# Kernel tuning notes

Measured on AMD Instinct MI355X. Metric: run time of the kernel, lower is better.

## Reference

```python
import jax, jax.numpy as jnp
import numpy as np

B, S, D, H = 2, 4096, 512, 8
DK = D // H
NEG = -9e15


def setup_inputs() -> dict:
    key = jax.random.key(0)
    ks = jax.random.split(key, 8)
    scale = 1.0 / np.sqrt(D)
    return {
        "q": jax.random.normal(ks[0], (B, S, D), jnp.float32),
        "k": jax.random.normal(ks[1], (B, S, D), jnp.float32),
        "v": jax.random.normal(ks[2], (B, S, D), jnp.float32),
        "mask": jnp.ones((1, 1, S, S), jnp.int32),
        "w_q": jax.random.normal(ks[3], (D, D), jnp.float32) * scale,
        "w_k": jax.random.normal(ks[4], (D, D), jnp.float32) * scale,
        "w_v": jax.random.normal(ks[5], (D, D), jnp.float32) * scale,
        "w_o": jax.random.normal(ks[6], (D, D), jnp.float32) * scale,
        "b_o": jnp.zeros((D,), jnp.float32),
    }


def reference(q, k, v, mask, w_q, w_k, w_v, w_o, b_o):
    # projections (nn.Linear: x @ W.T); split heads -> [B, H, S, DK]
    def split(x, w):
        return (x @ w.T).reshape(B, S, H, DK).transpose(0, 2, 1, 3)

    qh, kh, vh = split(q, w_q), split(k, w_k), split(v, w_v)
    scores = jnp.einsum("bhqd,bhkd->bhqk", qh, kh) / np.sqrt(DK)
    scores = jnp.where(mask == 0, NEG, scores)
    attn = jax.nn.softmax(scores, axis=-1)  # dropout p=0.0 (eval)
    out = jnp.einsum("bhqk,bhkd->bhqd", attn, vh)
    out = out.transpose(0, 2, 1, 3).reshape(B, S, D)
    return out @ w_o.T + b_o
```

## Files before the change

### kernel.cpp

```cpp
#include <hip/hip_runtime.h>
#include <hip/hip_fp16.h>

typedef _Float16 f16;
typedef _Float16 f16x2 __attribute__((ext_vector_type(2)));
typedef _Float16 f16x4v __attribute__((ext_vector_type(4)));
typedef _Float16 f16x8 __attribute__((ext_vector_type(8)));
typedef float f32x4 __attribute__((ext_vector_type(4)));
typedef float f32x16 __attribute__((ext_vector_type(16)));
typedef float fvec4 __attribute__((ext_vector_type(4)));
typedef unsigned int uint4v __attribute__((ext_vector_type(4)));

typedef f16x8 f16x8m __attribute__((may_alias));
typedef f16x4v f16x4m __attribute__((may_alias));

static constexpr int BB = 2, SS = 4096, DD = 512, HH = 8, DKK = 64;
static constexpr int MM = BB * SS;
static constexpr int NSPLIT = 2;
static constexpr int KVB = 32;
static constexpr int NT2 = SS / NSPLIT / KVB;
static constexpr float LOG2E = 1.4426950408889634f;
static constexpr float SMAX = 12.0f;

#define MFMA_F16(a, b, c) __builtin_amdgcn_mfma_f32_16x16x32_f16((a), (b), (c), 0, 0, 0)
#define MFMA32(a, b, c) __builtin_amdgcn_mfma_f32_32x32x16_f16((a), (b), (c), 0, 0, 0)

#define CVT_PKU(a, b) __builtin_bit_cast(unsigned, __builtin_amdgcn_cvt_pkrtz((a), (b)))

#define GLOAD16(gp, lp)                                                        \
  __builtin_amdgcn_global_load_lds(                                            \
      (const __attribute__((address_space(1))) void*)(const void*)(gp),        \
      (__attribute__((address_space(3))) void*)(lp), 16, 0, 0)

__global__ __launch_bounds__(256, 2) void proj3(
    const float* __restrict__ Aq, const float* __restrict__ Ak,
    const float* __restrict__ Av, const float* __restrict__ Wq,
    const float* __restrict__ Wk, const float* __restrict__ Wv,
    f16* __restrict__ Oq, f16* __restrict__ Ok, f16* __restrict__ Ov,
    float alq) {
  __shared__ __align__(16) f16 Al[2][128 * 32];
  __shared__ __align__(16) f16 Bl[2][128 * 32];

  const float* A32;
  const float* W;
  f16* Outp;
  float alpha;
  if (blockIdx.z == 0) {
    A32 = Aq; W = Wq; Outp = Oq; alpha = alq;
  } else if (blockIdx.z == 1) {
    A32 = Ak; W = Wk; Outp = Ok; alpha = 1.0f;
  } else {
    A32 = Av; W = Wv; Outp = Ov; alpha = 1.0f;
  }

  const int tid = threadIdx.x;
  const int lane = tid & 63;
  const int wave = tid >> 6;
  const int wm = wave >> 1, wn = wave & 1;
  const int cq = lane & 15, g = lane >> 4;
  const int bm = blockIdx.x, bn = blockIdx.y;

  f16x8 ar[2], br[2];

  auto loadStage = [&](int ks) {
#pragma unroll
    for (int i = 0; i < 2; ++i) {
      const int c = tid + 256 * i;
      const int row = c >> 2, cc = c & 3;
      const int k = ks * 32 + cc * 8;
      const float* p = A32 + (size_t)(bm * 128 + row) * DD + k;
      fvec4 x0 = *(const fvec4*)p;
      fvec4 x1 = *(const fvec4*)(p + 4);
      f16x8 h;
#pragma unroll
      for (int j = 0; j < 4; ++j) { h[j] = (f16)x0[j]; h[4 + j] = (f16)x1[j]; }
      ar[i] = h;
      const float* wp = W + (size_t)(bn * 128 + row) * DD + k;
      fvec4 y0 = *(const fvec4*)wp;
      fvec4 y1 = *(const fvec4*)(wp + 4);
      f16x8 hw;
#pragma unroll
      for (int j = 0; j < 4; ++j) { hw[j] = (f16)y0[j]; hw[4 + j] = (f16)y1[j]; }
      br[i] = hw;
    }
  };
  auto writeStage = [&](int bf) {
#pragma unroll
    for (int i = 0; i < 2; ++i) {
      const int c = tid + 256 * i;
      const int row = c >> 2, cc = c & 3;
      const int off = row * 32 + ((cc ^ (row & 3)) * 8);
      *(f16x8m*)&Al[bf][off] = ar[i];
      *(f16x8m*)&Bl[bf][off] = br[i];
    }
  };

  f32x4 acc[4][4] = {};
  loadStage(0);
  writeStage(0);
  __syncthreads();

  for (int ks = 0; ks < 16; ++ks) {
    const int bf = ks & 1;
    if (ks < 15) loadStage(ks + 1);
    f16x8 af[4], bfr[4];
#pragma unroll
    for (int f = 0; f < 4; ++f) {
      const int arow = wm * 64 + f * 16 + cq;
      af[f] = *(const f16x8m*)&Al[bf][arow * 32 + ((g ^ (arow & 3)) * 8)];
      const int brow = wn * 64 + f * 16 + cq;
      bfr[f] = *(const f16x8m*)&Bl[bf][brow * 32 + ((g ^ (brow & 3)) * 8)];
    }
#pragma unroll
    for (int fm = 0; fm < 4; ++fm)
#pragma unroll
      for (int fn = 0; fn < 4; ++fn)
        acc[fm][fn] = MFMA_F16(af[fm], bfr[fn], acc[fm][fn]);
    if (ks < 15) writeStage(bf ^ 1);
    __syncthreads();
  }

  const int rowb = bm * 128 + wm * 64;
  const int colb = bn * 128 + wn * 64;
#pragma unroll
  for (int fn = 0; fn < 4; ++fn) {
    const int col = colb + fn * 16 + cq;
#pragma unroll
    for (int fm = 0; fm < 4; ++fm) {
      const f32x4 v = acc[fm][fn];
#pragma unroll
      for (int r = 0; r < 4; ++r) {
        const int row = rowb + fm * 16 + 4 * g + r;
        const int b = row >> 12, s = row & 4095;
        const int h = col >> 6, dk = col & 63;
        Outp[(((size_t)(b * HH + h)) * SS + s) * DKK + dk] = (f16)(v[r] * alpha);
      }
    }
  }
}

__global__ __launch_bounds__(256, 2) void gemm_out(const f16* __restrict__ A16,
                                                   const float* __restrict__ W,
                                                   float* __restrict__ Out,
                                                   const float* __restrict__ bias) {
  __shared__ __align__(16) f16 Al[2][128 * 32];
  __shared__ __align__(16) f16 Bl[2][128 * 32];

  const int tid = threadIdx.x;
  const int lane = tid & 63;
  const int wave = tid >> 6;
  const int wm = wave >> 1, wn = wave & 1;
  const int cq = lane & 15, g = lane >> 4;
  const int bm = blockIdx.x, bn = blockIdx.y;

  f16x8 ar[2], br[2];
  auto loadStage = [&](int ks) {
#pragma unroll
    for (int i = 0; i < 2; ++i) {
      const int c = tid + 256 * i;
      const int row = c >> 2, cc = c & 3;
      const int k = ks * 32 + cc * 8;
      ar[i] = *(const f16x8*)(A16 + (size_t)(bm * 128 + row) * DD + k);
      const float* wp = W + (size_t)(bn * 128 + row) * DD + k;
      fvec4 y0 = *(const fvec4*)wp;
      fvec4 y1 = *(const fvec4*)(wp + 4);
      f16x8 hw;
#pragma unroll
      for (int j = 0; j < 4; ++j) { hw[j] = (f16)y0[j]; hw[4 + j] = (f16)y1[j]; }
      br[i] = hw;
    }
  };
  auto writeStage = [&](int bf) {
#pragma unroll
    for (int i = 0; i < 2; ++i) {
      const int c = tid + 256 * i;
      const int row = c >> 2, cc = c & 3;
      const int off = row * 32 + ((cc ^ (row & 3)) * 8);
      *(f16x8m*)&Al[bf][off] = ar[i];
      *(f16x8m*)&Bl[bf][off] = br[i];
    }
  };

  f32x4 acc[4][4] = {};
  loadStage(0);
  writeStage(0);
  __syncthreads();

  for (int ks = 0; ks < 16; ++ks) {
    const int bf = ks & 1;
    if (ks < 15) loadStage(ks + 1);
    f16x8 af[4], bfr[4];
#pragma unroll
    for (int f = 0; f < 4; ++f) {
      const int arow = wm * 64 + f * 16 + cq;
      af[f] = *(const f16x8m*)&Al[bf][arow * 32 + ((g ^ (arow & 3)) * 8)];
      const int brow = wn * 64 + f * 16 + cq;
      bfr[f] = *(const f16x8m*)&Bl[bf][brow * 32 + ((g ^ (brow & 3)) * 8)];
    }
#pragma unroll
    for (int fm = 0; fm < 4; ++fm)
#pragma unroll
      for (int fn = 0; fn < 4; ++fn)
        acc[fm][fn] = MFMA_F16(af[fm], bfr[fn], acc[fm][fn]);
    if (ks < 15) writeStage(bf ^ 1);
    __syncthreads();
  }

  const int rowb = bm * 128 + wm * 64;
  const int colb = bn * 128 + wn * 64;
#pragma unroll
  for (int fn = 0; fn < 4; ++fn) {
    const int col = colb + fn * 16 + cq;
    const float bb = bias[col];
#pragma unroll
    for (int fm = 0; fm < 4; ++fm) {
      const f32x4 v = acc[fm][fn];
#pragma unroll
      for (int r = 0; r < 4; ++r) {
        const int row = rowb + fm * 16 + 4 * g + r;
        Out[(size_t)row * DD + col] = v[r] + bb;
      }
    }
  }
}

__global__ __launch_bounds__(256) void transpose_v(const f16* __restrict__ Vh,
                                                   f16* __restrict__ Vt) {
  __shared__ __align__(16) f16 T[64][72];
  const int tid = threadIdx.x;
  const int bh = blockIdx.y;
  const int s0 = blockIdx.x * 64;
#pragma unroll
  for (int i = 0; i < 2; ++i) {
    const int c = tid + 256 * i;
    const int r = c >> 3, ch = c & 7;
    f16x8 v = *(const f16x8*)(Vh + ((size_t)bh * SS + s0 + r) * DKK + ch * 8);
#pragma unroll
    for (int j = 0; j < 8; ++j) T[r][ch * 8 + j] = v[j];
  }
  __syncthreads();
#pragma unroll
  for (int i = 0; i < 2; ++i) {
    const int c = tid + 256 * i;
    const int d = c >> 3, ch = c & 7;
    f16x4v lo, hi4;
#pragma unroll
    for (int j = 0; j < 4; ++j) lo[j] = T[ch * 8 + j][d];
#pragma unroll
    for (int j = 0; j < 4; ++j) hi4[j] = T[ch * 8 + 4 + j][d];
    f16* dst = Vt + ((size_t)bh * DKK + d) * SS + s0 + 16 * (ch >> 1) + 4 * (ch & 1);
    *(f16x4m*)dst = lo;
    *(f16x4m*)(dst + 8) = hi4;
  }
}

__global__ __launch_bounds__(256, 2) void attn_fwd(const f16* __restrict__ Qh,
                                                   const f16* __restrict__ Kh,
                                                   const f16* __restrict__ Vt,
                                                   f16* __restrict__ O) {
  __shared__ __align__(16) char smem[65536];

  const int tid = threadIdx.x, lane = tid & 63, wave = tid >> 6;
  const int q32 = lane & 31, hi = lane >> 5;
  const int e = wave & 1;
  const int sp = wave >> 1;
  const int bh = blockIdx.x & 15;
  const int qi = blockIdx.x >> 4;
  const int qrow0 = qi * 128 + e * 64;

  const f16* Qb = Qh + (size_t)bh * SS * DKK;
  const f16* Kb = Kh + (size_t)bh * SS * DKK;
  const f16* Vb = Vt + (size_t)bh * DKK * SS;

  char* const pb = smem + wave * 16384;
  f16* const pb16 = (f16*)pb;

  f16x8 qf0[4], qf1[4];
#pragma unroll
  for (int s = 0; s < 4; ++s) {
    qf0[s] = *(const f16x8*)(Qb + (size_t)(qrow0 + q32) * DKK + s * 16 + hi * 8);
    qf1[s] =
        *(const f16x8*)(Qb + (size_t)(qrow0 + 32 + q32) * DKK + s * 16 + hi * 8);
  }

  const f16* kRd[4];
#pragma unroll
  for (int s = 0; s < 4; ++s)
    kRd[s] = (const f16*)(pb + q32 * 128 + (((2 * s + hi) ^ (q32 & 7)) * 16));
  const f16* vRdA[2];
  const f16* vRdB[2];
#pragma unroll
  for (int s = 0; s < 2; ++s) {
    vRdA[s] = (const f16*)(pb + 8192 + q32 * 64 + (((2 * s + hi) ^ (q32 & 3)) * 16));
    vRdB[s] =
        (const f16*)(pb + 8192 + (32 + q32) * 64 + (((2 * s + hi) ^ (q32 & 3)) * 16));
  }

  const int rsub = lane >> 3;
  const int jsrc = (lane & 7) ^ rsub;
  const int r16 = lane >> 2;
  const int jsrcV = (lane & 3) ^ (r16 & 3);
  const int kvb0 = sp * (SS / NSPLIT);

  const f16* kS = Kb + (size_t)(kvb0 + rsub) * DKK + jsrc * 8;
  const f16* vS = Vb + (size_t)r16 * SS + kvb0 + jsrcV * 8;

  f16* const kDst = pb16;
  f16* const vDst = pb16 + 4096;

  auto stage = [&](int par) {
#pragma unroll
    for (int i = 0; i < 4; ++i)
      GLOAD16(kS + (size_t)i * 8 * DKK, kDst + par + i * 512);
#pragma unroll
    for (int i = 0; i < 4; ++i)
      GLOAD16(vS + (size_t)i * 16 * SS, vDst + par + i * 512);
    kS += KVB * DKK;
    vS += KVB;
  };

  f32x16 CINIT;
#pragma unroll
  for (int i = 0; i < 16; ++i) CINIT[i] = -SMAX;
  const f16 one1 = (f16)1.0f;
  const f16x8 ones = {one1, one1, one1, one1, one1, one1, one1, one1};

  f32x16 oacc00 = {}, oacc01 = {};
  f32x16 oacc10 = {}, oacc11 = {};
  f32x16 lacc0 = {}, lacc1 = {};

  struct PF { f16x8 s[2]; };
  PF pf0, pf1;

  stage(0);

  auto body = [&](int kt, int par) {
    if (kt < NT2 - 1) {
      stage(par ^ 2048);
      asm volatile("s_waitcnt vmcnt(8)" ::: "memory");
    } else {
      asm volatile("s_waitcnt vmcnt(0)" ::: "memory");
    }

    __builtin_amdgcn_s_setprio(1);
    f16x8 kf0 = *(const f16x8m*)(kRd[0] + par);
    f16x8 kf1 = *(const f16x8m*)(kRd[1] + par);
    f16x8 kf2 = *(const f16x8m*)(kRd[2] + par);
    f16x8 kf3 = *(const f16x8m*)(kRd[3] + par);
    f32x16 sc0 = MFMA32(kf0, qf0[0], CINIT);
    f32x16 sc1 = MFMA32(kf0, qf1[0], CINIT);
    sc0 = MFMA32(kf1, qf0[1], sc0);
    sc1 = MFMA32(kf1, qf1[1], sc1);
    sc0 = MFMA32(kf2, qf0[2], sc0);
    sc1 = MFMA32(kf2, qf1[2], sc1);
    sc0 = MFMA32(kf3, qf0[3], sc0);
    sc1 = MFMA32(kf3, qf1[3], sc1);
    __builtin_amdgcn_s_setprio(0);

#pragma unroll
    for (int i = 0; i < 16; ++i) sc0[i] = __builtin_amdgcn_exp2f(sc0[i]);
    unsigned dw[4];
#pragma unroll
    for (int s = 0; s < 2; ++s) {
#pragma unroll
      for (int m = 0; m < 4; ++m) {
        const int u = 2 * s + (m >> 1), c = m & 1;
        dw[m] = CVT_PKU(sc0[4 * u + 2 * c], sc0[4 * u + 2 * c + 1]);
      }
      uint4v uu = {dw[0], dw[1], dw[2], dw[3]};
      pf0.s[s] = __builtin_bit_cast(f16x8, uu);
    }
#pragma unroll
    for (int i = 0; i < 16; ++i) sc1[i] = __builtin_amdgcn_exp2f(sc1[i]);
#pragma unroll
    for (int s = 0; s < 2; ++s) {
#pragma unroll
      for (int m = 0; m < 4; ++m) {
        const int u = 2 * s + (m >> 1), c = m & 1;
        dw[m] = CVT_PKU(sc1[4 * u + 2 * c], sc1[4 * u + 2 * c + 1]);
      }
      uint4v uu = {dw[0], dw[1], dw[2], dw[3]};
      pf1.s[s] = __builtin_bit_cast(f16x8, uu);
    }

    __builtin_amdgcn_s_setprio(1);
#pragma unroll
    for (int s = 0; s < 2; ++s) {
      const f16x8 vA = *(const f16x8m*)(vRdA[s] + par);
      const f16x8 vB = *(const f16x8m*)(vRdB[s] + par);
      oacc00 = MFMA32(vA, pf0.s[s], oacc00);
      oacc01 = MFMA32(vB, pf0.s[s], oacc01);
      oacc10 = MFMA32(vA, pf1.s[s], oacc10);
      oacc11 = MFMA32(vB, pf1.s[s], oacc11);
      lacc0 = MFMA32(ones, pf0.s[s], lacc0);
      lacc1 = MFMA32(ones, pf1.s[s], lacc1);
    }
    __builtin_amdgcn_s_setprio(0);
  };

  for (int t = 0; t < NT2 / 2; ++t) {
    body(2 * t, 0);
    body(2 * t + 1, 2048);
  }

  float lr0 = lacc0[0], lr1 = lacc1[0];
  __syncthreads();
  float* const cbuf = (float*)smem;
  const int ci = (e * 64 + lane) * 67;
  if (sp == 1) {
#pragma unroll
    for (int i = 0; i < 16; ++i) {
      cbuf[ci + i] = oacc00[i];
      cbuf[ci + 16 + i] = oacc01[i];
      cbuf[ci + 33 + i] = oacc10[i];
      cbuf[ci + 49 + i] = oacc11[i];
    }
    cbuf[ci + 32] = lr0;
    cbuf[ci + 65] = lr1;
  }
  __syncthreads();
  if (sp == 0) {
#pragma unroll
    for (int i = 0; i < 16; ++i) {
      oacc00[i] += cbuf[ci + i];
      oacc01[i] += cbuf[ci + 16 + i];
      oacc10[i] += cbuf[ci + 33 + i];
      oacc11[i] += cbuf[ci + 49 + i];
    }
    lr0 += cbuf[ci + 32];
    lr1 += cbuf[ci + 65];

    const float inv0 = 1.f / lr0;
    const float inv1 = 1.f / lr1;
    const int b = bh >> 3, h = bh & 7;
#pragma unroll
    for (int g = 0; g < 2; ++g) {
      const float inv = g ? inv1 : inv0;
      const f32x16& oa = g ? oacc10 : oacc00;
      const f32x16& ob = g ? oacc11 : oacc01;
      const int srow = qrow0 + g * 32 + q32;
      f16* Orow = O + ((size_t)(b * SS + srow)) * DD + h * DKK;
#pragma unroll
      for (int u = 0; u < 4; ++u) {
        f16x4v o0, o1;
#pragma unroll
        for (int r = 0; r < 4; ++r) {
          o0[r] = (f16)(oa[4 * u + r] * inv);
          o1[r] = (f16)(ob[4 * u + r] * inv);
        }
        *(f16x4m*)(Orow + 8 * u + 4 * hi) = o0;
        *(f16x4m*)(Orow + 32 + 8 * u + 4 * hi) = o1;
      }
    }
  }
}

extern "C" void kernel_launch(void* const* d_in, const int* in_sizes, int n_in,
                              void* d_out, int out_size, void* d_ws,
                              size_t ws_size, hipStream_t stream) {
  const float* q = (const float*)d_in[0];
  const float* k = (const float*)d_in[1];
  const float* v = (const float*)d_in[2];
  const float* w_q = (const float*)d_in[4];
  const float* w_k = (const float*)d_in[5];
  const float* w_v = (const float*)d_in[6];
  const float* w_o = (const float*)d_in[7];
  const float* b_o = (const float*)d_in[8];
  float* out = (float*)d_out;

  char* ws = (char*)d_ws;
  const size_t SZ = (size_t)MM * DD * sizeof(f16);
  f16* Qh = (f16*)(ws + 0 * SZ);
  f16* Kh = (f16*)(ws + 1 * SZ);
  f16* Vh = (f16*)(ws + 2 * SZ);
  f16* Vt = (f16*)(ws + 3 * SZ);
  f16* Ob = (f16*)(ws + 4 * SZ);

  proj3<<<dim3(MM / 128, DD / 128, 3), 256, 0, stream>>>(
      q, k, v, w_q, w_k, w_v, Qh, Kh, Vh, 0.125f * LOG2E);
  transpose_v<<<dim3(SS / 64, BB * HH), 256, 0, stream>>>(Vh, Vt);
  attn_fwd<<<dim3(32 * BB * HH), 256, 0, stream>>>(Qh, Kh, Vt, Ob);
  gemm_out<<<dim3(MM / 128, DD / 128), 256, 0, stream>>>(Ob, w_o, out, b_o);
}
```

Baseline: 141.5 us.

## Share K/V LDS tiles between wave pairs and process two tiles per barrier

```diff
diff --git a/kernel.cpp b/kernel.cpp
--- a/kernel.cpp
+++ b/kernel.cpp
@@ -271,7 +271,7 @@
   const f16* Kb = Kh + (size_t)bh * SS * DKK;
   const f16* Vb = Vt + (size_t)bh * DKK * SS;
 
-  char* const pb = smem + wave * 16384;
+  char* const pb = smem + sp * 32768;
   f16* const pb16 = (f16*)pb;
 
   f16x8 qf0[4], qf1[4];
@@ -290,9 +290,10 @@
   const f16* vRdB[2];
 #pragma unroll
   for (int s = 0; s < 2; ++s) {
-    vRdA[s] = (const f16*)(pb + 8192 + q32 * 64 + (((2 * s + hi) ^ (q32 & 3)) * 16));
-    vRdB[s] =
-        (const f16*)(pb + 8192 + (32 + q32) * 64 + (((2 * s + hi) ^ (q32 & 3)) * 16));
+    vRdA[s] =
+        (const f16*)(pb + 16384 + q32 * 64 + (((2 * s + hi) ^ (q32 & 3)) * 16));
+    vRdB[s] = (const f16*)(pb + 16384 + (32 + q32) * 64 +
+                           (((2 * s + hi) ^ (q32 & 3)) * 16));
   }
 
   const int rsub = lane >> 3;
@@ -301,19 +302,19 @@
   const int jsrcV = (lane & 3) ^ (r16 & 3);
   const int kvb0 = sp * (SS / NSPLIT);
 
-  const f16* kS = Kb + (size_t)(kvb0 + rsub) * DKK + jsrc * 8;
-  const f16* vS = Vb + (size_t)r16 * SS + kvb0 + jsrcV * 8;
-
-  f16* const kDst = pb16;
-  f16* const vDst = pb16 + 4096;
-
-  auto stage = [&](int par) {
-#pragma unroll
-    for (int i = 0; i < 4; ++i)
-      GLOAD16(kS + (size_t)i * 8 * DKK, kDst + par + i * 512);
-#pragma unroll
-    for (int i = 0; i < 4; ++i)
-      GLOAD16(vS + (size_t)i * 16 * SS, vDst + par + i * 512);
+  const f16* kS = Kb + (size_t)(kvb0 + e * 16 + rsub) * DKK + jsrc * 8;
+  const f16* vS = Vb + (size_t)(e * 32 + r16) * SS + kvb0 + jsrcV * 8;
+
+  f16* const kDst0 = pb16 + (e * 16) * 64;
+  f16* const kDst1 = pb16 + (e * 16 + 8) * 64;
+  f16* const vDst0 = pb16 + 8192 + (e * 32) * 32;
+  f16* const vDst1 = pb16 + 8192 + (e * 32 + 16) * 32;
+
+  auto stage = [&](int slot) {
+    GLOAD16(kS, kDst0 + slot);
+    GLOAD16(kS + 8 * DKK, kDst1 + slot);
+    GLOAD16(vS, vDst0 + slot);
+    GLOAD16(vS + 16 * SS, vDst1 + slot);
     kS += KVB * DKK;
     vS += KVB;
   };
@@ -328,78 +329,109 @@
   f32x16 oacc10 = {}, oacc11 = {};
   f32x16 lacc0 = {}, lacc1 = {};
 
-  struct PF { f16x8 s[2]; };
-  PF pf0, pf1;
-
-  stage(0);
-
-  auto body = [&](int kt, int par) {
-    if (kt < NT2 - 1) {
-      stage(par ^ 2048);
-      asm volatile("s_waitcnt vmcnt(8)" ::: "memory");
-    } else {
-      asm volatile("s_waitcnt vmcnt(0)" ::: "memory");
-    }
-
-    __builtin_amdgcn_s_setprio(1);
-    f16x8 kf0 = *(const f16x8m*)(kRd[0] + par);
-    f16x8 kf1 = *(const f16x8m*)(kRd[1] + par);
-    f16x8 kf2 = *(const f16x8m*)(kRd[2] + par);
-    f16x8 kf3 = *(const f16x8m*)(kRd[3] + par);
-    f32x16 sc0 = MFMA32(kf0, qf0[0], CINIT);
-    f32x16 sc1 = MFMA32(kf0, qf1[0], CINIT);
-    sc0 = MFMA32(kf1, qf0[1], sc0);
-    sc1 = MFMA32(kf1, qf1[1], sc1);
-    sc0 = MFMA32(kf2, qf0[2], sc0);
-    sc1 = MFMA32(kf2, qf1[2], sc1);
-    sc0 = MFMA32(kf3, qf0[3], sc0);
-    sc1 = MFMA32(kf3, qf1[3], sc1);
-    __builtin_amdgcn_s_setprio(0);
-
-#pragma unroll
-    for (int i = 0; i < 16; ++i) sc0[i] = __builtin_amdgcn_exp2f(sc0[i]);
+  auto softpack = [&](f32x16& sc, f16x8* pf) {
+#pragma unroll
+    for (int i = 0; i < 16; ++i) sc[i] = __builtin_amdgcn_exp2f(sc[i]);
     unsigned dw[4];
 #pragma unroll
     for (int s = 0; s < 2; ++s) {
 #pragma unroll
       for (int m = 0; m < 4; ++m) {
         const int u = 2 * s + (m >> 1), c = m & 1;
-        dw[m] = CVT_PKU(sc0[4 * u + 2 * c], sc0[4 * u + 2 * c + 1]);
+        dw[m] = CVT_PKU(sc[4 * u + 2 * c], sc[4 * u + 2 * c + 1]);
       }
       uint4v uu = {dw[0], dw[1], dw[2], dw[3]};
-      pf0.s[s] = __builtin_bit_cast(f16x8, uu);
-    }
-#pragma unroll
-    for (int i = 0; i < 16; ++i) sc1[i] = __builtin_amdgcn_exp2f(sc1[i]);
+      pf[s] = __builtin_bit_cast(f16x8, uu);
+    }
+  };
+
+  stage(0);
+  stage(2048);
+  __syncthreads();
+
+  auto super = [&](int t, int par) {
+    const int opar = par ^ 4096;
+    if (t < NT2 / 2 - 1) {
+      stage(opar);
+      stage(opar + 2048);
+    }
+    const int pA = par, pB = par + 2048;
+
+    __builtin_amdgcn_s_setprio(1);
+    f32x16 scA0, scA1;
+    {
+      const f16x8 k0 = *(const f16x8m*)(kRd[0] + pA);
+      const f16x8 k1 = *(const f16x8m*)(kRd[1] + pA);
+      const f16x8 k2 = *(const f16x8m*)(kRd[2] + pA);
+      const f16x8 k3 = *(const f16x8m*)(kRd[3] + pA);
+      scA0 = MFMA32(k0, qf0[0], CINIT);
+      scA1 = MFMA32(k0, qf1[0], CINIT);
+      scA0 = MFMA32(k1, qf0[1], scA0);
+      scA1 = MFMA32(k1, qf1[1], scA1);
+      scA0 = MFMA32(k2, qf0[2], scA0);
+      scA1 = MFMA32(k2, qf1[2], scA1);
+      scA0 = MFMA32(k3, qf0[3], scA0);
+      scA1 = MFMA32(k3, qf1[3], scA1);
+    }
+    f32x16 scB0, scB1;
+    {
+      const f16x8 k0 = *(const f16x8m*)(kRd[0] + pB);
+      const f16x8 k1 = *(const f16x8m*)(kRd[1] + pB);
+      const f16x8 k2 = *(const f16x8m*)(kRd[2] + pB);
+      const f16x8 k3 = *(const f16x8m*)(kRd[3] + pB);
+      scB0 = MFMA32(k0, qf0[0], CINIT);
+      scB1 = MFMA32(k0, qf1[0], CINIT);
+      scB0 = MFMA32(k1, qf0[1], scB0);
+      scB1 = MFMA32(k1, qf1[1], scB1);
+      scB0 = MFMA32(k2, qf0[2], scB0);
+      scB1 = MFMA32(k2, qf1[2], scB1);
+      scB0 = MFMA32(k3, qf0[3], scB0);
+      scB1 = MFMA32(k3, qf1[3], scB1);
+    }
+    __builtin_amdgcn_s_setprio(0);
+
+    f16x8 pfA0[2], pfA1[2];
+    softpack(scA0, pfA0);
+    softpack(scA1, pfA1);
+
+    __builtin_amdgcn_s_setprio(1);
 #pragma unroll
     for (int s = 0; s < 2; ++s) {
-#pragma unroll
-      for (int m = 0; m < 4; ++m) {
-        const int u = 2 * s + (m >> 1), c = m & 1;
-        dw[m] = CVT_PKU(sc1[4 * u + 2 * c], sc1[4 * u + 2 * c + 1]);
-      }
-      uint4v uu = {dw[0], dw[1], dw[2], dw[3]};
-      pf1.s[s] = __builtin_bit_cast(f16x8, uu);
-    }
+      const f16x8 vA = *(const f16x8m*)(vRdA[s] + pA);
+      const f16x8 vB = *(const f16x8m*)(vRdB[s] + pA);
+      oacc00 = MFMA32(vA, pfA0[s], oacc00);
+      oacc01 = MFMA32(vB, pfA0[s], oacc01);
+      oacc10 = MFMA32(vA, pfA1[s], oacc10);
+      oacc11 = MFMA32(vB, pfA1[s], oacc11);
+      lacc0 = MFMA32(ones, pfA0[s], lacc0);
+      lacc1 = MFMA32(ones, pfA1[s], lacc1);
+    }
+    __builtin_amdgcn_s_setprio(0);
+
+    f16x8 pfB0[2], pfB1[2];
+    softpack(scB0, pfB0);
+    softpack(scB1, pfB1);
 
     __builtin_amdgcn_s_setprio(1);
 #pragma unroll
     for (int s = 0; s < 2; ++s) {
-      const f16x8 vA = *(const f16x8m*)(vRdA[s] + par);
-      const f16x8 vB = *(const f16x8m*)(vRdB[s] + par);
-      oacc00 = MFMA32(vA, pf0.s[s], oacc00);
-      oacc01 = MFMA32(vB, pf0.s[s], oacc01);
-      oacc10 = MFMA32(vA, pf1.s[s], oacc10);
-      oacc11 = MFMA32(vB, pf1.s[s], oacc11);
-      lacc0 = MFMA32(ones, pf0.s[s], lacc0);
-      lacc1 = MFMA32(ones, pf1.s[s], lacc1);
+      const f16x8 vA = *(const f16x8m*)(vRdA[s] + pB);
+      const f16x8 vB = *(const f16x8m*)(vRdB[s] + pB);
+      oacc00 = MFMA32(vA, pfB0[s], oacc00);
+      oacc01 = MFMA32(vB, pfB0[s], oacc01);
+      oacc10 = MFMA32(vA, pfB1[s], oacc10);
+      oacc11 = MFMA32(vB, pfB1[s], oacc11);
+      lacc0 = MFMA32(ones, pfB0[s], lacc0);
+      lacc1 = MFMA32(ones, pfB1[s], lacc1);
     }
     __builtin_amdgcn_s_setprio(0);
-  };
-
-  for (int t = 0; t < NT2 / 2; ++t) {
-    body(2 * t, 0);
-    body(2 * t + 1, 2048);
+
+    __syncthreads();
+  };
+
+  for (int tt = 0; tt < NT2 / 4; ++tt) {
+    super(2 * tt, 0);
+    super(2 * tt + 1, 4096);
   }
 
   float lr0 = lacc0[0], lr1 = lacc1[0];
```

New measurement: 133.8 us. 1.06x faster.

## Load K/V tiles directly into registers and compute row sums with VALU

Applied to the files above, without the earlier changes.

```diff
diff --git a/kernel.cpp b/kernel.cpp
--- a/kernel.cpp
+++ b/kernel.cpp
@@ -9,6 +9,7 @@
 typedef float f32x16 __attribute__((ext_vector_type(16)));
 typedef float fvec4 __attribute__((ext_vector_type(4)));
 typedef unsigned int uint4v __attribute__((ext_vector_type(4)));
+typedef unsigned int uint2v __attribute__((ext_vector_type(2)));
 
 typedef f16x8 f16x8m __attribute__((may_alias));
 typedef f16x4v f16x4m __attribute__((may_alias));
@@ -25,11 +26,6 @@
 #define MFMA32(a, b, c) __builtin_amdgcn_mfma_f32_32x32x16_f16((a), (b), (c), 0, 0, 0)
 
 #define CVT_PKU(a, b) __builtin_bit_cast(unsigned, __builtin_amdgcn_cvt_pkrtz((a), (b)))
-
-#define GLOAD16(gp, lp)                                                        \
-  __builtin_amdgcn_global_load_lds(                                            \
-      (const __attribute__((address_space(1))) void*)(const void*)(gp),        \
-      (__attribute__((address_space(3))) void*)(lp), 16, 0, 0)
 
 __global__ __launch_bounds__(256, 2) void proj3(
     const float* __restrict__ Aq, const float* __restrict__ Ak,
@@ -257,7 +253,7 @@
                                                    const f16* __restrict__ Kh,
                                                    const f16* __restrict__ Vt,
                                                    f16* __restrict__ O) {
-  __shared__ __align__(16) char smem[65536];
+  __shared__ __align__(16) float cbuf[128 * 67];
 
   const int tid = threadIdx.x, lane = tid & 63, wave = tid >> 6;
   const int q32 = lane & 31, hi = lane >> 5;
@@ -271,9 +267,6 @@
   const f16* Kb = Kh + (size_t)bh * SS * DKK;
   const f16* Vb = Vt + (size_t)bh * DKK * SS;
 
-  char* const pb = smem + wave * 16384;
-  f16* const pb16 = (f16*)pb;
-
   f16x8 qf0[4], qf1[4];
 #pragma unroll
   for (int s = 0; s < 4; ++s) {
@@ -282,129 +275,105 @@
         *(const f16x8*)(Qb + (size_t)(qrow0 + 32 + q32) * DKK + s * 16 + hi * 8);
   }
 
-  const f16* kRd[4];
-#pragma unroll
-  for (int s = 0; s < 4; ++s)
-    kRd[s] = (const f16*)(pb + q32 * 128 + (((2 * s + hi) ^ (q32 & 7)) * 16));
-  const f16* vRdA[2];
-  const f16* vRdB[2];
-#pragma unroll
-  for (int s = 0; s < 2; ++s) {
-    vRdA[s] = (const f16*)(pb + 8192 + q32 * 64 + (((2 * s + hi) ^ (q32 & 3)) * 16));
-    vRdB[s] =
-        (const f16*)(pb + 8192 + (32 + q32) * 64 + (((2 * s + hi) ^ (q32 & 3)) * 16));
-  }
-
-  const int rsub = lane >> 3;
-  const int jsrc = (lane & 7) ^ rsub;
-  const int r16 = lane >> 2;
-  const int jsrcV = (lane & 3) ^ (r16 & 3);
   const int kvb0 = sp * (SS / NSPLIT);
-
-  const f16* kS = Kb + (size_t)(kvb0 + rsub) * DKK + jsrc * 8;
-  const f16* vS = Vb + (size_t)r16 * SS + kvb0 + jsrcV * 8;
-
-  f16* const kDst = pb16;
-  f16* const vDst = pb16 + 4096;
-
-  auto stage = [&](int par) {
-#pragma unroll
-    for (int i = 0; i < 4; ++i)
-      GLOAD16(kS + (size_t)i * 8 * DKK, kDst + par + i * 512);
-#pragma unroll
-    for (int i = 0; i < 4; ++i)
-      GLOAD16(vS + (size_t)i * 16 * SS, vDst + par + i * 512);
-    kS += KVB * DKK;
-    vS += KVB;
+  const f16* kP = Kb + (size_t)(kvb0 + q32) * DKK + hi * 8;
+  const f16* vPA = Vb + (size_t)q32 * SS + kvb0 + hi * 8;
+  const f16* vPB = Vb + (size_t)(32 + q32) * SS + kvb0 + hi * 8;
+
+  struct KV {
+    f16x8 k[4];
+    f16x8 v[4];
+  };
+  auto loadKV = [&]() -> KV {
+    KV t;
+#pragma unroll
+    for (int s = 0; s < 4; ++s) t.k[s] = *(const f16x8m*)(kP + s * 16);
+#pragma unroll
+    for (int s = 0; s < 2; ++s) {
+      t.v[s] = *(const f16x8m*)(vPA + s * 16);
+      t.v[2 + s] = *(const f16x8m*)(vPB + s * 16);
+    }
+    kP += KVB * DKK;
+    vPA += KVB;
+    vPB += KVB;
+    return t;
   };
 
   f32x16 CINIT;
 #pragma unroll
   for (int i = 0; i < 16; ++i) CINIT[i] = -SMAX;
-  const f16 one1 = (f16)1.0f;
-  const f16x8 ones = {one1, one1, one1, one1, one1, one1, one1, one1};
 
   f32x16 oacc00 = {}, oacc01 = {};
   f32x16 oacc10 = {}, oacc11 = {};
-  f32x16 lacc0 = {}, lacc1 = {};
-
-  struct PF { f16x8 s[2]; };
-  PF pf0, pf1;
-
-  stage(0);
-
-  auto body = [&](int kt, int par) {
-    if (kt < NT2 - 1) {
-      stage(par ^ 2048);
-      asm volatile("s_waitcnt vmcnt(8)" ::: "memory");
-    } else {
-      asm volatile("s_waitcnt vmcnt(0)" ::: "memory");
-    }
-
-    __builtin_amdgcn_s_setprio(1);
-    f16x8 kf0 = *(const f16x8m*)(kRd[0] + par);
-    f16x8 kf1 = *(const f16x8m*)(kRd[1] + par);
-    f16x8 kf2 = *(const f16x8m*)(kRd[2] + par);
-    f16x8 kf3 = *(const f16x8m*)(kRd[3] + par);
-    f32x16 sc0 = MFMA32(kf0, qf0[0], CINIT);
-    f32x16 sc1 = MFMA32(kf0, qf1[0], CINIT);
-    sc0 = MFMA32(kf1, qf0[1], sc0);
-    sc1 = MFMA32(kf1, qf1[1], sc1);
-    sc0 = MFMA32(kf2, qf0[2], sc0);
-    sc1 = MFMA32(kf2, qf1[2], sc1);
-    sc0 = MFMA32(kf3, qf0[3], sc0);
-    sc1 = MFMA32(kf3, qf1[3], sc1);
-    __builtin_amdgcn_s_setprio(0);
-
-#pragma unroll
-    for (int i = 0; i < 16; ++i) sc0[i] = __builtin_amdgcn_exp2f(sc0[i]);
-    unsigned dw[4];
+  float lr0 = 0.f, lr1 = 0.f;
+
+  auto softpack = [&](f32x16 sc, f16x8* pf, float& lrun) {
+#pragma unroll
+    for (int i = 0; i < 16; ++i) sc[i] = __builtin_amdgcn_exp2f(sc[i]);
+    unsigned dwa[2][4];
 #pragma unroll
     for (int s = 0; s < 2; ++s) {
 #pragma unroll
       for (int m = 0; m < 4; ++m) {
         const int u = 2 * s + (m >> 1), c = m & 1;
-        dw[m] = CVT_PKU(sc0[4 * u + 2 * c], sc0[4 * u + 2 * c + 1]);
+        dwa[s][m] = CVT_PKU(sc[4 * u + 2 * c], sc[4 * u + 2 * c + 1]);
       }
-      uint4v uu = {dw[0], dw[1], dw[2], dw[3]};
-      pf0.s[s] = __builtin_bit_cast(f16x8, uu);
-    }
-#pragma unroll
-    for (int i = 0; i < 16; ++i) sc1[i] = __builtin_amdgcn_exp2f(sc1[i]);
+      uint4v uu = {dwa[s][0], dwa[s][1], dwa[s][2], dwa[s][3]};
+      pf[s] = __builtin_bit_cast(f16x8, uu);
+    }
+    const f16x2 t0 = __builtin_bit_cast(f16x2, dwa[0][0]) +
+                     __builtin_bit_cast(f16x2, dwa[0][1]);
+    const f16x2 t1 = __builtin_bit_cast(f16x2, dwa[0][2]) +
+                     __builtin_bit_cast(f16x2, dwa[0][3]);
+    const f16x2 t2 = __builtin_bit_cast(f16x2, dwa[1][0]) +
+                     __builtin_bit_cast(f16x2, dwa[1][1]);
+    const f16x2 t3 = __builtin_bit_cast(f16x2, dwa[1][2]) +
+                     __builtin_bit_cast(f16x2, dwa[1][3]);
+    const f16x2 tt = (t0 + t1) + (t2 + t3);
+    float ts = (float)tt[0] + (float)tt[1];
+    uint2v rs = __builtin_amdgcn_permlane32_swap(
+        __builtin_bit_cast(unsigned, ts), __builtin_bit_cast(unsigned, ts),
+        false, false);
+    ts += __builtin_bit_cast(float, hi ? rs[0] : rs[1]);
+    lrun += ts;
+  };
+
+  auto compute = [&](const KV& t) {
+    __builtin_amdgcn_s_setprio(1);
+    f32x16 sc0 = MFMA32(t.k[0], qf0[0], CINIT);
+    f32x16 sc1 = MFMA32(t.k[0], qf1[0], CINIT);
+    sc0 = MFMA32(t.k[1], qf0[1], sc0);
+    sc1 = MFMA32(t.k[1], qf1[1], sc1);
+    sc0 = MFMA32(t.k[2], qf0[2], sc0);
+    sc1 = MFMA32(t.k[2], qf1[2], sc1);
+    sc0 = MFMA32(t.k[3], qf0[3], sc0);
+    sc1 = MFMA32(t.k[3], qf1[3], sc1);
+    __builtin_amdgcn_s_setprio(0);
+
+    f16x8 pf0[2], pf1[2];
+    softpack(sc0, pf0, lr0);
+    softpack(sc1, pf1, lr1);
+
+    __builtin_amdgcn_s_setprio(1);
 #pragma unroll
     for (int s = 0; s < 2; ++s) {
-#pragma unroll
-      for (int m = 0; m < 4; ++m) {
-        const int u = 2 * s + (m >> 1), c = m & 1;
-        dw[m] = CVT_PKU(sc1[4 * u + 2 * c], sc1[4 * u + 2 * c + 1]);
-      }
-      uint4v uu = {dw[0], dw[1], dw[2], dw[3]};
-      pf1.s[s] = __builtin_bit_cast(f16x8, uu);
-    }
-
-    __builtin_amdgcn_s_setprio(1);
-#pragma unroll
-    for (int s = 0; s < 2; ++s) {
-      const f16x8 vA = *(const f16x8m*)(vRdA[s] + par);
-      const f16x8 vB = *(const f16x8m*)(vRdB[s] + par);
-      oacc00 = MFMA32(vA, pf0.s[s], oacc00);
-      oacc01 = MFMA32(vB, pf0.s[s], oacc01);
-      oacc10 = MFMA32(vA, pf1.s[s], oacc10);
-      oacc11 = MFMA32(vB, pf1.s[s], oacc11);
-      lacc0 = MFMA32(ones, pf0.s[s], lacc0);
-      lacc1 = MFMA32(ones, pf1.s[s], lacc1);
+      oacc00 = MFMA32(t.v[s], pf0[s], oacc00);
+      oacc01 = MFMA32(t.v[2 + s], pf0[s], oacc01);
+      oacc10 = MFMA32(t.v[s], pf1[s], oacc10);
+      oacc11 = MFMA32(t.v[2 + s], pf1[s], oacc11);
     }
     __builtin_amdgcn_s_setprio(0);
   };
 
+  KV curA = loadKV();
   for (int t = 0; t < NT2 / 2; ++t) {
-    body(2 * t, 0);
-    body(2 * t + 1, 2048);
-  }
-
-  float lr0 = lacc0[0], lr1 = lacc1[0];
+    KV curB = loadKV();
+    compute(curA);
+    if (t < NT2 / 2 - 1) curA = loadKV();
+    compute(curB);
+  }
+
   __syncthreads();
-  float* const cbuf = (float*)smem;
   const int ci = (e * 64 + lane) * 67;
   if (sp == 1) {
 #pragma unroll
```

New measurement: 173.5 us. 22.6% more time.

## Share 64-key K/V tiles across wave pairs and compute row sums with packed adds

Applied to the files above, without the earlier changes.

```diff
diff --git a/kernel.cpp b/kernel.cpp
--- a/kernel.cpp
+++ b/kernel.cpp
@@ -9,6 +9,7 @@
 typedef float f32x16 __attribute__((ext_vector_type(16)));
 typedef float fvec4 __attribute__((ext_vector_type(4)));
 typedef unsigned int uint4v __attribute__((ext_vector_type(4)));
+typedef unsigned int uint2v __attribute__((ext_vector_type(2)));
 
 typedef f16x8 f16x8m __attribute__((may_alias));
 typedef f16x4v f16x4m __attribute__((may_alias));
@@ -16,8 +17,8 @@
 static constexpr int BB = 2, SS = 4096, DD = 512, HH = 8, DKK = 64;
 static constexpr int MM = BB * SS;
 static constexpr int NSPLIT = 2;
-static constexpr int KVB = 32;
-static constexpr int NT2 = SS / NSPLIT / KVB;
+static constexpr int KVB = 64;
+static constexpr int NT3 = SS / NSPLIT / KVB;
 static constexpr float LOG2E = 1.4426950408889634f;
 static constexpr float SMAX = 12.0f;
 
@@ -271,7 +272,7 @@
   const f16* Kb = Kh + (size_t)bh * SS * DKK;
   const f16* Vb = Vt + (size_t)bh * DKK * SS;
 
-  char* const pb = smem + wave * 16384;
+  char* const pb = smem + sp * 32768;
   f16* const pb16 = (f16*)pb;
 
   f16x8 qf0[4], qf1[4];
@@ -282,30 +283,24 @@
         *(const f16x8*)(Qb + (size_t)(qrow0 + 32 + q32) * DKK + s * 16 + hi * 8);
   }
 
-  const f16* kRd[4];
+  const f16* kRdLo[4];
 #pragma unroll
   for (int s = 0; s < 4; ++s)
-    kRd[s] = (const f16*)(pb + q32 * 128 + (((2 * s + hi) ^ (q32 & 7)) * 16));
-  const f16* vRdA[2];
-  const f16* vRdB[2];
-#pragma unroll
-  for (int s = 0; s < 2; ++s) {
-    vRdA[s] = (const f16*)(pb + 8192 + q32 * 64 + (((2 * s + hi) ^ (q32 & 3)) * 16));
-    vRdB[s] =
-        (const f16*)(pb + 8192 + (32 + q32) * 64 + (((2 * s + hi) ^ (q32 & 3)) * 16));
-  }
+    kRdLo[s] = pb16 + q32 * 64 + ((2 * s + hi) ^ (q32 & 7)) * 8;
+  const f16* vRdA[4];
+#pragma unroll
+  for (int t = 0; t < 4; ++t)
+    vRdA[t] = pb16 + 8192 + q32 * 64 + ((2 * t + hi) ^ (q32 & 7)) * 8;
 
   const int rsub = lane >> 3;
   const int jsrc = (lane & 7) ^ rsub;
-  const int r16 = lane >> 2;
-  const int jsrcV = (lane & 3) ^ (r16 & 3);
   const int kvb0 = sp * (SS / NSPLIT);
 
-  const f16* kS = Kb + (size_t)(kvb0 + rsub) * DKK + jsrc * 8;
-  const f16* vS = Vb + (size_t)r16 * SS + kvb0 + jsrcV * 8;
-
-  f16* const kDst = pb16;
-  f16* const vDst = pb16 + 4096;
+  const f16* kS = Kb + (size_t)(kvb0 + e * 32 + rsub) * DKK + jsrc * 8;
+  const f16* vS = Vb + (size_t)(e * 32 + rsub) * SS + kvb0 + jsrc * 8;
+
+  f16* const kDst = pb16 + e * 2048;
+  f16* const vDst = pb16 + 8192 + e * 2048;
 
   auto stage = [&](int par) {
 #pragma unroll
@@ -313,96 +308,124 @@
       GLOAD16(kS + (size_t)i * 8 * DKK, kDst + par + i * 512);
 #pragma unroll
     for (int i = 0; i < 4; ++i)
-      GLOAD16(vS + (size_t)i * 16 * SS, vDst + par + i * 512);
-    kS += KVB * DKK;
+      GLOAD16(vS + (size_t)i * 8 * SS, vDst + par + i * 512);
+    kS += (size_t)KVB * DKK;
     vS += KVB;
   };
 
   f32x16 CINIT;
 #pragma unroll
   for (int i = 0; i < 16; ++i) CINIT[i] = -SMAX;
-  const f16 one1 = (f16)1.0f;
-  const f16x8 ones = {one1, one1, one1, one1, one1, one1, one1, one1};
 
   f32x16 oacc00 = {}, oacc01 = {};
   f32x16 oacc10 = {}, oacc11 = {};
-  f32x16 lacc0 = {}, lacc1 = {};
-
-  struct PF { f16x8 s[2]; };
-  PF pf0, pf1;
+  float lr0 = 0.f, lr1 = 0.f;
+
+  auto packg = [&](f32x16 sLo, f32x16 sHi, f16x8* pf, float& lr) {
+#pragma unroll
+    for (int i = 0; i < 16; ++i) sLo[i] = __builtin_amdgcn_exp2f(sLo[i]);
+#pragma unroll
+    for (int i = 0; i < 16; ++i) sHi[i] = __builtin_amdgcn_exp2f(sHi[i]);
+    unsigned da[4], db[4], dc[4], dd[4];
+#pragma unroll
+    for (int m = 0; m < 4; ++m) {
+      const int u = m >> 1, c = m & 1;
+      da[m] = CVT_PKU(sLo[4 * u + 2 * c], sLo[4 * u + 2 * c + 1]);
+      db[m] = CVT_PKU(sLo[4 * (u + 2) + 2 * c], sLo[4 * (u + 2) + 2 * c + 1]);
+      dc[m] = CVT_PKU(sHi[4 * u + 2 * c], sHi[4 * u + 2 * c + 1]);
+      dd[m] = CVT_PKU(sHi[4 * (u + 2) + 2 * c], sHi[4 * (u + 2) + 2 * c + 1]);
+    }
+    {
+      uint4v u0 = {da[0], da[1], da[2], da[3]};
+      uint4v u1 = {db[0], db[1], db[2], db[3]};
+      uint4v u2 = {dc[0], dc[1], dc[2], dc[3]};
+      uint4v u3 = {dd[0], dd[1], dd[2], dd[3]};
+      pf[0] = __builtin_bit_cast(f16x8, u0);
+      pf[1] = __builtin_bit_cast(f16x8, u1);
+      pf[2] = __builtin_bit_cast(f16x8, u2);
+      pf[3] = __builtin_bit_cast(f16x8, u3);
+    }
+    const f16x2 t0 = (__builtin_bit_cast(f16x2, da[0]) + __builtin_bit_cast(f16x2, da[1])) +
+                     (__builtin_bit_cast(f16x2, da[2]) + __builtin_bit_cast(f16x2, da[3]));
+    const f16x2 t1 = (__builtin_bit_cast(f16x2, db[0]) + __builtin_bit_cast(f16x2, db[1])) +
+                     (__builtin_bit_cast(f16x2, db[2]) + __builtin_bit_cast(f16x2, db[3]));
+    const f16x2 t2 = (__builtin_bit_cast(f16x2, dc[0]) + __builtin_bit_cast(f16x2, dc[1])) +
+                     (__builtin_bit_cast(f16x2, dc[2]) + __builtin_bit_cast(f16x2, dc[3]));
+    const f16x2 t3 = (__builtin_bit_cast(f16x2, dd[0]) + __builtin_bit_cast(f16x2, dd[1])) +
+                     (__builtin_bit_cast(f16x2, dd[2]) + __builtin_bit_cast(f16x2, dd[3]));
+    const f16x2 tt = (t0 + t1) + (t2 + t3);
+    lr += (float)tt[0] + (float)tt[1];
+  };
 
   stage(0);
+  __syncthreads();
 
   auto body = [&](int kt, int par) {
-    if (kt < NT2 - 1) {
-      stage(par ^ 2048);
-      asm volatile("s_waitcnt vmcnt(8)" ::: "memory");
-    } else {
-      asm volatile("s_waitcnt vmcnt(0)" ::: "memory");
-    }
+    if (kt < NT3 - 1) stage(par ^ 4096);
 
     __builtin_amdgcn_s_setprio(1);
-    f16x8 kf0 = *(const f16x8m*)(kRd[0] + par);
-    f16x8 kf1 = *(const f16x8m*)(kRd[1] + par);
-    f16x8 kf2 = *(const f16x8m*)(kRd[2] + par);
-    f16x8 kf3 = *(const f16x8m*)(kRd[3] + par);
-    f32x16 sc0 = MFMA32(kf0, qf0[0], CINIT);
-    f32x16 sc1 = MFMA32(kf0, qf1[0], CINIT);
-    sc0 = MFMA32(kf1, qf0[1], sc0);
-    sc1 = MFMA32(kf1, qf1[1], sc1);
-    sc0 = MFMA32(kf2, qf0[2], sc0);
-    sc1 = MFMA32(kf2, qf1[2], sc1);
-    sc0 = MFMA32(kf3, qf0[3], sc0);
-    sc1 = MFMA32(kf3, qf1[3], sc1);
+    f16x8 kLo[4], kHi[4];
+#pragma unroll
+    for (int s = 0; s < 4; ++s) {
+      kLo[s] = *(const f16x8m*)(kRdLo[s] + par);
+      kHi[s] = *(const f16x8m*)(kRdLo[s] + 2048 + par);
+    }
+    f32x16 sLo0 = MFMA32(kLo[0], qf0[0], CINIT);
+    f32x16 sHi0 = MFMA32(kHi[0], qf0[0], CINIT);
+    f32x16 sLo1 = MFMA32(kLo[0], qf1[0], CINIT);
+    f32x16 sHi1 = MFMA32(kHi[0], qf1[0], CINIT);
+#pragma unroll
+    for (int s = 1; s < 4; ++s) {
+      sLo0 = MFMA32(kLo[s], qf0[s], sLo0);
+      sHi0 = MFMA32(kHi[s], qf0[s], sHi0);
+      sLo1 = MFMA32(kLo[s], qf1[s], sLo1);
+      sHi1 = MFMA32(kHi[s], qf1[s], sHi1);
+    }
     __builtin_amdgcn_s_setprio(0);
 
-#pragma unroll
-    for (int i = 0; i < 16; ++i) sc0[i] = __builtin_amdgcn_exp2f(sc0[i]);
-    unsigned dw[4];
-#pragma unroll
-    for (int s = 0; s < 2; ++s) {
-#pragma unroll
-      for (int m = 0; m < 4; ++m) {
-        const int u = 2 * s + (m >> 1), c = m & 1;
-        dw[m] = CVT_PKU(sc0[4 * u + 2 * c], sc0[4 * u + 2 * c + 1]);
-      }
-      uint4v uu = {dw[0], dw[1], dw[2], dw[3]};
-      pf0.s[s] = __builtin_bit_cast(f16x8, uu);
-    }
-#pragma unroll
-    for (int i = 0; i < 16; ++i) sc1[i] = __builtin_amdgcn_exp2f(sc1[i]);
-#pragma unroll
-    for (int s = 0; s < 2; ++s) {
-#pragma unroll
-      for (int m = 0; m < 4; ++m) {
-        const int u = 2 * s + (m >> 1), c = m & 1;
-        dw[m] = CVT_PKU(sc1[4 * u + 2 * c], sc1[4 * u + 2 * c + 1]);
-      }
-      uint4v uu = {dw[0], dw[1], dw[2], dw[3]};
-      pf1.s[s] = __builtin_bit_cast(f16x8, uu);
-    }
-
+    f16x8 vA[4], vB[4];
+#pragma unroll
+    for (int t = 0; t < 4; ++t) {
+      vA[t] = *(const f16x8m*)(vRdA[t] + par);
+      vB[t] = *(const f16x8m*)(vRdA[t] + 2048 + par);
+    }
+
+    f16x8 pf[4];
+    packg(sLo0, sHi0, pf, lr0);
+#pragma unroll
+    for (int t = 0; t < 4; ++t) {
+      oacc00 = MFMA32(vA[t], pf[t], oacc00);
+      oacc01 = MFMA32(vB[t], pf[t], oacc01);
+    }
+
+    packg(sLo1, sHi1, pf, lr1);
     __builtin_amdgcn_s_setprio(1);
 #pragma unroll
-    for (int s = 0; s < 2; ++s) {
-      const f16x8 vA = *(const f16x8m*)(vRdA[s] + par);
-      const f16x8 vB = *(const f16x8m*)(vRdB[s] + par);
-      oacc00 = MFMA32(vA, pf0.s[s], oacc00);
-      oacc01 = MFMA32(vB, pf0.s[s], oacc01);
-      oacc10 = MFMA32(vA, pf1.s[s], oacc10);
-      oacc11 = MFMA32(vB, pf1.s[s], oacc11);
-      lacc0 = MFMA32(ones, pf0.s[s], lacc0);
-      lacc1 = MFMA32(ones, pf1.s[s], lacc1);
+    for (int t = 0; t < 4; ++t) {
+      oacc10 = MFMA32(vA[t], pf[t], oacc10);
+      oacc11 = MFMA32(vB[t], pf[t], oacc11);
     }
     __builtin_amdgcn_s_setprio(0);
-  };
-
-  for (int t = 0; t < NT2 / 2; ++t) {
+
+    __syncthreads();
+  };
+
+  for (int t = 0; t < NT3 / 2; ++t) {
     body(2 * t, 0);
-    body(2 * t + 1, 2048);
-  }
-
-  float lr0 = lacc0[0], lr1 = lacc1[0];
+    body(2 * t + 1, 4096);
+  }
+
+  {
+    uint2v rs = __builtin_amdgcn_permlane32_swap(
+        __builtin_bit_cast(unsigned, lr0), __builtin_bit_cast(unsigned, lr0),
+        false, false);
+    lr0 += __builtin_bit_cast(float, hi ? rs[0] : rs[1]);
+    uint2v rt = __builtin_amdgcn_permlane32_swap(
+        __builtin_bit_cast(unsigned, lr1), __builtin_bit_cast(unsigned, lr1),
+        false, false);
+    lr1 += __builtin_bit_cast(float, hi ? rt[0] : rt[1]);
+  }
+
   __syncthreads();
   float* const cbuf = (float*)smem;
   const int ci = (e * 64 + lane) * 67;
```

Result: faster. 124.9 us (-11.7%).
